# Performance work log

Hardware: AMD Instinct MI355X
Metric: run time of the kernel (lower is better)

## Reference

```python
import jax, jax.numpy as jnp
import numpy as np

DIST = 3.0
COEFF = 10.0
NEG_SLOPE = 0.3  # keras LeakyReLU default


def _probe_points(dist=DIST):
    # fixed 26 probe offsets on a sphere of radius `dist` (from build())
    angles = np.array(
        [[j * 0.125 - 0.125, i * 0.125 + (j - 1) * 0.0625] for j in range(3) for i in range(8)]
        + [[-0.25, 0.0], [0.25, 0.0]],
        dtype=np.float32,
    ) * (2.0 * np.pi)
    a, b = angles[:, 0], angles[:, 1]
    pts = np.stack([np.sin(a), np.cos(a) * np.cos(b), np.cos(a) * np.sin(b)], axis=-1) * dist
    return jnp.asarray(pts, dtype=jnp.float32)  # (26, 3)


def setup_inputs() -> dict:
    key = jax.random.key(0)
    k1, k2, k3 = jax.random.split(key, 3)
    B, n, f = 2, 1024, 3
    m, out_feats, num_convs = 26, 6, 5
    points = jax.random.normal(k1, (B, n, 3 + f), dtype=jnp.float32)
    # per-conv Dense(m*f -> out_feats) weights/bias, stacked over num_convs
    W = jax.random.normal(k2, (num_convs, m * f, out_feats), dtype=jnp.float32) * 0.1
    b = jax.random.normal(k3, (num_convs, out_feats), dtype=jnp.float32) * 0.1
    return {"points": points, "W": W, "b": b}


def reference(points, W, b):
    B, n, df = points.shape
    d = 3
    f = df - d
    probes = _probe_points()              # (m, d)
    m = probes.shape[0]
    coords = points[..., :d]              # (B, n, d) -> centers too (l = n)
    feats = points[..., d:]               # (B, n, f)
    centers = coords
    # probes per center: (B, l, m, d)
    probes_per_center = centers[:, :, None, :] + probes[None, None, :, :]
    # delta: (B, l, m, n, d)
    delta = coords[:, None, None, :, :] - probes_per_center[:, :, :, None, :]
    sq = jnp.sum(delta * delta, axis=-1)  # (B, l, m, n)
    wgt = COEFF / (sq + COEFF)            # inverse-distance weights
    # weighted feature sum: (B, l, m, f), averaged over n
    wf = jnp.einsum('blmn,bnf->blmf', wgt, feats) / n
    x = wf.reshape(B, n, m * f)           # (B, l, m*f)
    # num_convs parallel Dense + LeakyReLU (Dropout is identity at inference)
    h = jnp.einsum('blx,kxo->blko', x, W) + b[None, None, :, :]
    h = jnp.where(h > 0, h, NEG_SLOPE * h)
    convs = h.reshape(B, n, -1)           # (B, n, num_convs*out_feats)
    return jnp.concatenate([centers, convs], axis=-1)  # (B, n, 3 + 30)
```

## Files before the change

kernel.cpp:

```cpp
#include <hip/hip_runtime.h>


#define NPTS   1024
#define COEFF  10.0f
#define NEG    0.3f

typedef float v2f __attribute__((ext_vector_type(2)));

__device__ __forceinline__ v2f pkfma(v2f a, v2f b, v2f c) {
#if __has_builtin(__builtin_elementwise_fma)
  return __builtin_elementwise_fma(a, b, c);
#else
  return v2f{fmaf(a.x, b.x, c.x), fmaf(a.y, b.y, c.y)};
#endif
}
__device__ __forceinline__ v2f splat(float s) { return v2f{s, s}; }

constexpr int M0[14] = {0,5, 1,4, 2,3, 7,6, 8,12, 10,14, 24,25};
constexpr int M1[12] = {16,19, 17,18, 20,23, 21,22, 9,13, 11,15};

#define DPP_STEP(x, ctrl, rm, bm, bc)                                        \
  x += __int_as_float(__builtin_amdgcn_update_dpp(                           \
      0, __float_as_int(x), ctrl, rm, bm, bc))

__device__ __forceinline__ float wave_sum_to_lane63(float x) {
  DPP_STEP(x, 0x111, 0xf, 0xf, true);
  DPP_STEP(x, 0x112, 0xf, 0xf, true);
  DPP_STEP(x, 0x114, 0xf, 0xe, false);
  DPP_STEP(x, 0x118, 0xf, 0xc, false);
  DPP_STEP(x, 0x142, 0xa, 0xf, false);
  DPP_STEP(x, 0x143, 0xc, 0xf, false);
  return x;
}

__device__ __forceinline__ void rcp4pk(v2f tA, v2f tB, v2f& wA, v2f& wB) {
  const float pA = tA.x * tA.y;
  const float pB = tB.x * tB.y;
  const float r  = __builtin_amdgcn_rcpf(pA * pB);
  const v2f  rp  = v2f{pB, pA} * r;
  wA = v2f{tA.y, tA.x} * rp.x;
  wB = v2f{tB.y, tB.x} * rp.y;
}
__device__ __forceinline__ v2f rcp2pk(v2f t) {
  const float r = __builtin_amdgcn_rcpf(t.x * t.y);
  return v2f{t.y, t.x} * r;
}

#define CA 4.24264068f
#define CY 3.91968890f
#define CZ 1.62358830f

template <int HALF>
__device__ void run_main(const float* __restrict__ batch, int lane,
                         float cx, float cy, float cz, v2f* a01, float* a2) {
  constexpr int NPAIR = HALF ? 6 : 7;
  #pragma unroll 2
  for (int it = 0; it < NPTS / 64; ++it) {
    const float* prow = batch + (it * 64 + lane) * 6;
    const float2 q0 = *reinterpret_cast<const float2*>(prow);
    const float2 q1 = *reinterpret_cast<const float2*>(prow + 2);
    const float2 q2 = *reinterpret_cast<const float2*>(prow + 4);
    const float dx = q0.x - cx, dy = q0.y - cy, dz = q1.x - cz;
    const v2f   f01 = {q1.y, q2.x};
    const float f2  = q2.y;
    const float base = fmaf(dx, dx, fmaf(dy, dy, fmaf(dz, dz, 19.0f)));

    v2f tp[7];
    if constexpr (HALF == 0) {
      const float rx = fmaf(CA, dx, base);
      const float sA = fmaf( CZ, dz, rx);
      const float sB = fmaf(-CZ, dz, rx);
      const float sC = fmaf(-CY, dz, rx);
      const float sD = fmaf( CY, dz, rx);
      tp[0] = pkfma(v2f{-CY,  CY}, splat(dy), splat(sA));
      tp[1] = pkfma(v2f{-CY,  CY}, splat(dy), splat(sB));
      tp[2] = pkfma(v2f{-CZ,  CZ}, splat(dy), splat(sC));
      tp[3] = pkfma(v2f{-CZ,  CZ}, splat(dy), splat(sD));
      tp[4] = pkfma(v2f{-6.f, 6.f}, splat(dy), splat(base));
      tp[5] = pkfma(v2f{-6.f, 6.f}, splat(dz), splat(base));
      tp[6] = pkfma(v2f{ 6.f,-6.f}, splat(dx), splat(base));
    } else {
      const float rx = fmaf(-CA, dx, base);
      const float sA = fmaf(-CZ, dz, rx);
      const float sB = fmaf(-CY, dz, rx);
      const float sC = fmaf( CZ, dz, rx);
      const float sD = fmaf( CY, dz, rx);
      tp[0] = pkfma(v2f{-CY,  CY}, splat(dy), splat(sA));
      tp[1] = pkfma(v2f{-CZ,  CZ}, splat(dy), splat(sB));
      tp[2] = pkfma(v2f{ CY, -CY}, splat(dy), splat(sC));
      tp[3] = pkfma(v2f{ CZ, -CZ}, splat(dy), splat(sD));
      const float u = dy + dz, v = dy - dz;
      tp[4] = pkfma(v2f{-CA,  CA}, splat(u), splat(base));
      tp[5] = pkfma(v2f{ CA, -CA}, splat(v), splat(base));
    }

    v2f wp[7];
    rcp4pk(tp[0], tp[1], wp[0], wp[1]);
    rcp4pk(tp[2], tp[3], wp[2], wp[3]);
    rcp4pk(tp[4], tp[5], wp[4], wp[5]);
    if constexpr (HALF == 0) wp[6] = rcp2pk(tp[6]);

    #pragma unroll
    for (int p = 0; p < NPAIR; ++p) {
      a01[2*p]     = pkfma(splat(wp[p].x), f01, a01[2*p]);
      a01[2*p + 1] = pkfma(splat(wp[p].y), f01, a01[2*p + 1]);
      a2[2*p]      = fmaf(wp[p].x, f2, a2[2*p]);
      a2[2*p + 1]  = fmaf(wp[p].y, f2, a2[2*p + 1]);
    }
  }
}

template <int HALF>
__device__ __forceinline__ void reduce_store(v2f* a01, float* a2, int lane,
                                             float* sx) {
  constexpr int NP = HALF ? 12 : 14;
  #pragma unroll
  for (int j = 0; j < NP; ++j) {
    a01[j].x = wave_sum_to_lane63(a01[j].x);
    a01[j].y = wave_sum_to_lane63(a01[j].y);
    a2[j]    = wave_sum_to_lane63(a2[j]);
  }
  if (lane == 63) {
    #pragma unroll
    for (int j = 0; j < NP; ++j) {
      const int m = HALF ? M1[j] : M0[j];
      sx[m * 3 + 0] = a01[j].x;
      sx[m * 3 + 1] = a01[j].y;
      sx[m * 3 + 2] = a2[j];
    }
  }
}

__global__ __launch_bounds__(256, 4) void crossconv_kernel(
    const float* __restrict__ points,
    const float* __restrict__ W,
    const float* __restrict__ bias,
    float* __restrict__ out)
{
    __shared__ __align__(16) float sx[2][80];

    const int tid    = threadIdx.x;
    const int lane   = tid & 63;
    const int w      = tid >> 6;
    const int cLocal = w >> 1;
    const int half   = w & 1;
    const int G      = blockIdx.x * 2 + cLocal;

    const float* batch = points + (G >> 10) * (NPTS * 6);
    const float* crow  = points + G * 6;
    const float  cx = crow[0], cy = crow[1], cz = crow[2];

    v2f   a01[14];
    float a2[14];
    #pragma unroll
    for (int j = 0; j < 14; ++j) { a01[j] = v2f{0.f, 0.f}; a2[j] = 0.f; }

    if (half == 0) run_main<0>(batch, lane, cx, cy, cz, a01, a2);
    else           run_main<1>(batch, lane, cx, cy, cz, a01, a2);

    if (half == 0) reduce_store<0>(a01, a2, lane, sx[cLocal]);
    else           reduce_store<1>(a01, a2, lane, sx[cLocal]);
    __syncthreads();

    if (half == 0) {
      const float scale = COEFF / (float)NPTS;
      float* orow = out + G * 33;
      if (lane < 30) {
        const int k = lane / 6, o = lane % 6;
        const float* Wk = W + k * (78 * 6) + o;
        float h0 = 0.f, h1 = 0.f, h2 = 0.f, h3 = 0.f;
        const float4* sxv = reinterpret_cast<const float4*>(sx[cLocal]);
        #pragma unroll
        for (int t4 = 0; t4 < 19; ++t4) {
          const float4 v = sxv[t4];
          h0 = fmaf(v.x, Wk[(t4 * 4 + 0) * 6], h0);
          h1 = fmaf(v.y, Wk[(t4 * 4 + 1) * 6], h1);
          h2 = fmaf(v.z, Wk[(t4 * 4 + 2) * 6], h2);
          h3 = fmaf(v.w, Wk[(t4 * 4 + 3) * 6], h3);
        }
        const float2 vt = *reinterpret_cast<const float2*>(&sx[cLocal][76]);
        h0 = fmaf(vt.x, Wk[76 * 6], h0);
        h1 = fmaf(vt.y, Wk[77 * 6], h1);
        const float dot = (h0 + h2) + (h1 + h3);
        float h = fmaf(dot, scale, bias[lane]);
        h = (h > 0.f) ? h : NEG * h;
        orow[3 + lane] = h;
      } else if (lane < 33) {
        orow[lane - 30] = (lane == 30) ? cx : ((lane == 31) ? cy : cz);
      }
    }
}

extern "C" void kernel_launch(void* const* d_in, const int* in_sizes, int n_in,
                              void* d_out, int out_size, void* d_ws, size_t ws_size,
                              hipStream_t stream) {
    const float* points = (const float*)d_in[0];
    const float* W      = (const float*)d_in[1];
    const float* bias   = (const float*)d_in[2];
    float* out          = (float*)d_out;
    crossconv_kernel<<<1024, 256, 0, stream>>>(points, W, bias, out);
}
```

Measured before the change: 23.84 us.

## Process two points per lane with fp16 packed dot2 accumulation

Each lane now handles two neighbor points per iteration, packing their coordinate math into 2-wide float vectors. The inverse-distance weights and features are converted to packed fp16, and accumulation uses v_dot2 (fp16 inputs, fp32 accumulator), so one instruction covers both points. The aim is fewer VALU instructions per point-probe pair. In exchange, weights and features lose precision to fp16 round-toward-zero. The old cross-probe reciprocal sharing is replaced by one rcp per probe that serves both points.

```diff
diff --git a/kernel.cpp b/kernel.cpp
--- a/kernel.cpp
+++ b/kernel.cpp
@@ -5,19 +5,23 @@
 #define COEFF  10.0f
 #define NEG    0.3f
 
-typedef float v2f __attribute__((ext_vector_type(2)));
+typedef float  v2f __attribute__((ext_vector_type(2)));
+typedef __fp16 h2  __attribute__((ext_vector_type(2)));
 
-__device__ __forceinline__ v2f pkfma(v2f a, v2f b, v2f c) {
-#if __has_builtin(__builtin_elementwise_fma)
-  return __builtin_elementwise_fma(a, b, c);
-#else
-  return v2f{fmaf(a.x, b.x, c.x), fmaf(a.y, b.y, c.y)};
-#endif
-}
-__device__ __forceinline__ v2f splat(float s) { return v2f{s, s}; }
+#define CA 4.24264068f
+#define CY 3.91968890f
+#define CZ 1.62358830f
 
 constexpr int M0[14] = {0,5, 1,4, 2,3, 7,6, 8,12, 10,14, 24,25};
 constexpr int M1[12] = {16,19, 17,18, 20,23, 21,22, 9,13, 11,15};
+
+__device__ __forceinline__ v2f vfma(float c, v2f a, v2f b) {
+#if __has_builtin(__builtin_elementwise_fma)
+  return __builtin_elementwise_fma(v2f{c, c}, a, b);
+#else
+  return v2f{fmaf(c, a.x, b.x), fmaf(c, a.y, b.y)};
+#endif
+}
 
 #define DPP_STEP(x, ctrl, rm, bm, bc)                                        \
   x += __int_as_float(__builtin_amdgcn_update_dpp(                           \
@@ -33,100 +37,89 @@
   return x;
 }
 
-__device__ __forceinline__ void rcp4pk(v2f tA, v2f tB, v2f& wA, v2f& wB) {
-  const float pA = tA.x * tA.y;
-  const float pB = tB.x * tB.y;
-  const float r  = __builtin_amdgcn_rcpf(pA * pB);
-  const v2f  rp  = v2f{pB, pA} * r;
-  wA = v2f{tA.y, tA.x} * rp.x;
-  wB = v2f{tB.y, tB.x} * rp.y;
+template <int HALF>
+__device__ __forceinline__ void tgen(v2f dx, v2f dy, v2f dz, v2f base, v2f* t) {
+  if constexpr (HALF == 0) {
+    const v2f rx = vfma( CA, dx, base);
+    const v2f sA = vfma( CZ, dz, rx);
+    const v2f sB = vfma(-CZ, dz, rx);
+    const v2f sC = vfma(-CY, dz, rx);
+    const v2f sD = vfma( CY, dz, rx);
+    t[0]  = vfma(-CY, dy, sA);   t[1]  = vfma( CY, dy, sA);
+    t[2]  = vfma(-CY, dy, sB);   t[3]  = vfma( CY, dy, sB);
+    t[4]  = vfma(-CZ, dy, sC);   t[5]  = vfma( CZ, dy, sC);
+    t[6]  = vfma(-CZ, dy, sD);   t[7]  = vfma( CZ, dy, sD);
+    t[8]  = vfma(-6.f, dy, base); t[9]  = vfma( 6.f, dy, base);
+    t[10] = vfma(-6.f, dz, base); t[11] = vfma( 6.f, dz, base);
+    t[12] = vfma( 6.f, dx, base); t[13] = vfma(-6.f, dx, base);
+  } else {
+    const v2f rx = vfma(-CA, dx, base);
+    const v2f sA = vfma(-CZ, dz, rx);
+    const v2f sB = vfma(-CY, dz, rx);
+    const v2f sC = vfma( CZ, dz, rx);
+    const v2f sD = vfma( CY, dz, rx);
+    const v2f u = dy + dz, v = dy - dz;
+    t[0]  = vfma(-CY, dy, sA);   t[1]  = vfma( CY, dy, sA);
+    t[2]  = vfma(-CZ, dy, sB);   t[3]  = vfma( CZ, dy, sB);
+    t[4]  = vfma( CY, dy, sC);   t[5]  = vfma(-CY, dy, sC);
+    t[6]  = vfma( CZ, dy, sD);   t[7]  = vfma(-CZ, dy, sD);
+    t[8]  = vfma(-CA, u, base);  t[9]  = vfma( CA, u, base);
+    t[10] = vfma( CA, v, base);  t[11] = vfma(-CA, v, base);
+  }
 }
-__device__ __forceinline__ v2f rcp2pk(v2f t) {
-  const float r = __builtin_amdgcn_rcpf(t.x * t.y);
-  return v2f{t.y, t.x} * r;
-}
-
-#define CA 4.24264068f
-#define CY 3.91968890f
-#define CZ 1.62358830f
 
 template <int HALF>
 __device__ void run_main(const float* __restrict__ batch, int lane,
-                         float cx, float cy, float cz, v2f* a01, float* a2) {
-  constexpr int NPAIR = HALF ? 6 : 7;
-  #pragma unroll 2
-  for (int it = 0; it < NPTS / 64; ++it) {
-    const float* prow = batch + (it * 64 + lane) * 6;
-    const float2 q0 = *reinterpret_cast<const float2*>(prow);
-    const float2 q1 = *reinterpret_cast<const float2*>(prow + 2);
-    const float2 q2 = *reinterpret_cast<const float2*>(prow + 4);
-    const float dx = q0.x - cx, dy = q0.y - cy, dz = q1.x - cz;
-    const v2f   f01 = {q1.y, q2.x};
-    const float f2  = q2.y;
-    const float base = fmaf(dx, dx, fmaf(dy, dy, fmaf(dz, dz, 19.0f)));
+                         float cx, float cy, float cz, float* acc) {
+  constexpr int NP = HALF ? 12 : 14;
+  for (int it = 0; it < NPTS / 128; ++it) {
+    const float* prowA = batch + (it * 128 + lane) * 6;
+    const float* prowB = prowA + 64 * 6;
+    const float2 a0 = *reinterpret_cast<const float2*>(prowA);
+    const float2 a1 = *reinterpret_cast<const float2*>(prowA + 2);
+    const float2 a2 = *reinterpret_cast<const float2*>(prowA + 4);
+    const float2 b0 = *reinterpret_cast<const float2*>(prowB);
+    const float2 b1 = *reinterpret_cast<const float2*>(prowB + 2);
+    const float2 b2 = *reinterpret_cast<const float2*>(prowB + 4);
 
-    v2f tp[7];
-    if constexpr (HALF == 0) {
-      const float rx = fmaf(CA, dx, base);
-      const float sA = fmaf( CZ, dz, rx);
-      const float sB = fmaf(-CZ, dz, rx);
-      const float sC = fmaf(-CY, dz, rx);
-      const float sD = fmaf( CY, dz, rx);
-      tp[0] = pkfma(v2f{-CY,  CY}, splat(dy), splat(sA));
-      tp[1] = pkfma(v2f{-CY,  CY}, splat(dy), splat(sB));
-      tp[2] = pkfma(v2f{-CZ,  CZ}, splat(dy), splat(sC));
-      tp[3] = pkfma(v2f{-CZ,  CZ}, splat(dy), splat(sD));
-      tp[4] = pkfma(v2f{-6.f, 6.f}, splat(dy), splat(base));
-      tp[5] = pkfma(v2f{-6.f, 6.f}, splat(dz), splat(base));
-      tp[6] = pkfma(v2f{ 6.f,-6.f}, splat(dx), splat(base));
-    } else {
-      const float rx = fmaf(-CA, dx, base);
-      const float sA = fmaf(-CZ, dz, rx);
-      const float sB = fmaf(-CY, dz, rx);
-      const float sC = fmaf( CZ, dz, rx);
-      const float sD = fmaf( CY, dz, rx);
-      tp[0] = pkfma(v2f{-CY,  CY}, splat(dy), splat(sA));
-      tp[1] = pkfma(v2f{-CZ,  CZ}, splat(dy), splat(sB));
-      tp[2] = pkfma(v2f{ CY, -CY}, splat(dy), splat(sC));
-      tp[3] = pkfma(v2f{ CZ, -CZ}, splat(dy), splat(sD));
-      const float u = dy + dz, v = dy - dz;
-      tp[4] = pkfma(v2f{-CA,  CA}, splat(u), splat(base));
-      tp[5] = pkfma(v2f{ CA, -CA}, splat(v), splat(base));
-    }
+    const v2f dx = v2f{a0.x, b0.x} - cx;
+    const v2f dy = v2f{a0.y, b0.y} - cy;
+    const v2f dz = v2f{a1.x, b1.x} - cz;
+    v2f base = vfma(1.f, dz * dz, v2f{19.f, 19.f});
+    base = __builtin_elementwise_fma(dy, dy, base);
+    base = __builtin_elementwise_fma(dx, dx, base);
 
-    v2f wp[7];
-    rcp4pk(tp[0], tp[1], wp[0], wp[1]);
-    rcp4pk(tp[2], tp[3], wp[2], wp[3]);
-    rcp4pk(tp[4], tp[5], wp[4], wp[5]);
-    if constexpr (HALF == 0) wp[6] = rcp2pk(tp[6]);
+    v2f t[NP];
+    tgen<HALF>(dx, dy, dz, base, t);
+
+    const h2 f0p = __builtin_amdgcn_cvt_pkrtz(a1.y, b1.y);
+    const h2 f1p = __builtin_amdgcn_cvt_pkrtz(a2.x, b2.x);
+    const h2 f2p = __builtin_amdgcn_cvt_pkrtz(a2.y, b2.y);
 
     #pragma unroll
-    for (int p = 0; p < NPAIR; ++p) {
-      a01[2*p]     = pkfma(splat(wp[p].x), f01, a01[2*p]);
-      a01[2*p + 1] = pkfma(splat(wp[p].y), f01, a01[2*p + 1]);
-      a2[2*p]      = fmaf(wp[p].x, f2, a2[2*p]);
-      a2[2*p + 1]  = fmaf(wp[p].y, f2, a2[2*p + 1]);
+    for (int j = 0; j < NP; ++j) {
+      const float r  = __builtin_amdgcn_rcpf(t[j].x * t[j].y);
+      const h2 wp = __builtin_amdgcn_cvt_pkrtz(t[j].y * r, t[j].x * r);
+      acc[j * 3 + 0] = __builtin_amdgcn_fdot2(wp, f0p, acc[j * 3 + 0], false);
+      acc[j * 3 + 1] = __builtin_amdgcn_fdot2(wp, f1p, acc[j * 3 + 1], false);
+      acc[j * 3 + 2] = __builtin_amdgcn_fdot2(wp, f2p, acc[j * 3 + 2], false);
     }
   }
 }
 
 template <int HALF>
-__device__ __forceinline__ void reduce_store(v2f* a01, float* a2, int lane,
-                                             float* sx) {
+__device__ __forceinline__ void reduce_store(float* acc, int lane, float* sx) {
   constexpr int NP = HALF ? 12 : 14;
   #pragma unroll
-  for (int j = 0; j < NP; ++j) {
-    a01[j].x = wave_sum_to_lane63(a01[j].x);
-    a01[j].y = wave_sum_to_lane63(a01[j].y);
-    a2[j]    = wave_sum_to_lane63(a2[j]);
-  }
+  for (int j = 0; j < NP * 3; ++j)
+    acc[j] = wave_sum_to_lane63(acc[j]);
   if (lane == 63) {
     #pragma unroll
     for (int j = 0; j < NP; ++j) {
       const int m = HALF ? M1[j] : M0[j];
-      sx[m * 3 + 0] = a01[j].x;
-      sx[m * 3 + 1] = a01[j].y;
-      sx[m * 3 + 2] = a2[j];
+      sx[m * 3 + 0] = acc[j * 3 + 0];
+      sx[m * 3 + 1] = acc[j * 3 + 1];
+      sx[m * 3 + 2] = acc[j * 3 + 2];
     }
   }
 }
@@ -150,16 +143,15 @@
     const float* crow  = points + G * 6;
     const float  cx = crow[0], cy = crow[1], cz = crow[2];
 
-    v2f   a01[14];
-    float a2[14];
+    float acc[42];
     #pragma unroll
-    for (int j = 0; j < 14; ++j) { a01[j] = v2f{0.f, 0.f}; a2[j] = 0.f; }
+    for (int j = 0; j < 42; ++j) acc[j] = 0.f;
 
-    if (half == 0) run_main<0>(batch, lane, cx, cy, cz, a01, a2);
-    else           run_main<1>(batch, lane, cx, cy, cz, a01, a2);
+    if (half == 0) run_main<0>(batch, lane, cx, cy, cz, acc);
+    else           run_main<1>(batch, lane, cx, cy, cz, acc);
 
-    if (half == 0) reduce_store<0>(a01, a2, lane, sx[cLocal]);
-    else           reduce_store<1>(a01, a2, lane, sx[cLocal]);
+    if (half == 0) reduce_store<0>(acc, lane, sx[cLocal]);
+    else           reduce_store<1>(acc, lane, sx[cLocal]);
     __syncthreads();
 
     if (half == 0) {
@@ -168,20 +160,20 @@
       if (lane < 30) {
         const int k = lane / 6, o = lane % 6;
         const float* Wk = W + k * (78 * 6) + o;
-        float h0 = 0.f, h1 = 0.f, h2 = 0.f, h3 = 0.f;
+        float h0 = 0.f, h1 = 0.f, h2_ = 0.f, h3 = 0.f;
         const float4* sxv = reinterpret_cast<const float4*>(sx[cLocal]);
         #pragma unroll
         for (int t4 = 0; t4 < 19; ++t4) {
           const float4 v = sxv[t4];
-          h0 = fmaf(v.x, Wk[(t4 * 4 + 0) * 6], h0);
-          h1 = fmaf(v.y, Wk[(t4 * 4 + 1) * 6], h1);
-          h2 = fmaf(v.z, Wk[(t4 * 4 + 2) * 6], h2);
-          h3 = fmaf(v.w, Wk[(t4 * 4 + 3) * 6], h3);
+          h0  = fmaf(v.x, Wk[(t4 * 4 + 0) * 6], h0);
+          h1  = fmaf(v.y, Wk[(t4 * 4 + 1) * 6], h1);
+          h2_ = fmaf(v.z, Wk[(t4 * 4 + 2) * 6], h2_);
+          h3  = fmaf(v.w, Wk[(t4 * 4 + 3) * 6], h3);
         }
         const float2 vt = *reinterpret_cast<const float2*>(&sx[cLocal][76]);
         h0 = fmaf(vt.x, Wk[76 * 6], h0);
         h1 = fmaf(vt.y, Wk[77 * 6], h1);
-        const float dot = (h0 + h2) + (h1 + h3);
+        const float dot = (h0 + h2_) + (h1 + h3);
         float h = fmaf(dot, scale, bias[lane]);
         h = (h > 0.f) ? h : NEG * h;
         orow[3 + lane] = h;
```

Measured after the change: 23.69 us. Within noise of the previous version (-0.6%).
